# Kernel optimization log

Hardware: AMD Instinct MI355X
Metric: run time of the kernel (lower is better)

## Reference

```python
import jax, jax.numpy as jnp
import numpy as np

HIDDEN = 768
NUM_HEADS = 12
HEAD_DIM = HIDDEN // NUM_HEADS


def setup_inputs() -> dict:
    key = jax.random.key(0)
    ks = jax.random.split(key, 10)
    B, S = 4, 2048
    scale = 1.0 / np.sqrt(HIDDEN)
    inp = {
        "hidden_states": jax.random.normal(ks[0], (B, S, HIDDEN), dtype=jnp.float32),
        "attention_mask": jnp.ones((B, S), dtype=jnp.float32),
        "Wq": jax.random.normal(ks[1], (HIDDEN, HIDDEN), dtype=jnp.float32) * scale,
        "bq": jnp.zeros((HIDDEN,), dtype=jnp.float32),
        "Wk": jax.random.normal(ks[2], (HIDDEN, HIDDEN), dtype=jnp.float32) * scale,
        "bk": jnp.zeros((HIDDEN,), dtype=jnp.float32),
        "Wv": jax.random.normal(ks[3], (HIDDEN, HIDDEN), dtype=jnp.float32) * scale,
        "bv": jnp.zeros((HIDDEN,), dtype=jnp.float32),
        "Wo": jax.random.normal(ks[4], (HIDDEN, HIDDEN), dtype=jnp.float32) * scale,
        "bo": jnp.zeros((HIDDEN,), dtype=jnp.float32),
    }
    return inp


def _split_heads(x):
    # [B,S,H] -> [B,nh,S,dh]
    B, S, _ = x.shape
    return x.reshape(B, S, NUM_HEADS, HEAD_DIM).transpose(0, 2, 1, 3)


def reference(hidden_states, attention_mask, Wq, bq, Wk, bk, Wv, bv, Wo, bo):
    # Linear projections (torch nn.Linear: x @ W.T + b; here W stored as [in,out])
    q = _split_heads(hidden_states @ Wq + bq)
    k = _split_heads(hidden_states @ Wk + bk)
    v = _split_heads(hidden_states @ Wv + bv)

    # scores: [B,nh,S,S]
    scores = jnp.einsum("bhqd,bhkd->bhqk", q, k) / np.sqrt(HEAD_DIM).astype(np.float32)

    # outer-product mask: [B,1,S,S], broadcast over heads
    ext = (attention_mask[:, :, None] * attention_mask[:, None, :])[:, None, :, :]
    scores = ext * scores - (1.0 - ext) * 1e9

    probs = jax.nn.softmax(scores, axis=-1)
    ctx = jnp.einsum("bhqk,bhkd->bhqd", probs, v)  # [B,nh,S,dh]
    B, _, S, _ = ctx.shape
    ctx = ctx.transpose(0, 2, 1, 3).reshape(B, S, HIDDEN)
    out = ctx @ Wo + bo
    # torch F.gelu default: exact (erf-based)
    return jax.nn.gelu(out, approximate=False)
```

## Files before the change

kernel.cpp:

```cpp
#include <hip/hip_runtime.h>
#include <math.h>

#define HIDDEN 768
#define NH 12
#define DH 64
#define SEQ 2048
#define BATCH 4

typedef __bf16 bf16;
typedef bf16 bf16x4 __attribute__((ext_vector_type(4)));
typedef bf16 bf16x8 __attribute__((ext_vector_type(8)));
typedef float f32x4 __attribute__((ext_vector_type(4)));

__device__ __forceinline__ void load_lds16(const void* g, void* l) {
    __builtin_amdgcn_global_load_lds(
        (__attribute__((address_space(1))) void*)g,
        (__attribute__((address_space(3))) void*)l, 16, 0, 0);
}

__global__ __launch_bounds__(256) void prep_x(const float* __restrict__ X,
                                              bf16* __restrict__ Xb) {
    const size_t i = ((size_t)blockIdx.x * 256 + threadIdx.x) * 8;
    float4 a = *(const float4*)(X + i);
    float4 b = *(const float4*)(X + i + 4);
    bf16x8 o = {(bf16)a.x, (bf16)a.y, (bf16)a.z, (bf16)a.w,
                (bf16)b.x, (bf16)b.y, (bf16)b.z, (bf16)b.w};
    *(bf16x8*)(Xb + i) = o;
}

__global__ __launch_bounds__(256) void prep_w(const float* __restrict__ Wq,
                                              const float* __restrict__ Wk,
                                              const float* __restrict__ Wv,
                                              const float* __restrict__ Wo,
                                              bf16* __restrict__ Wt,
                                              bf16* __restrict__ Wot_hi,
                                              bf16* __restrict__ Wot_lo) {
    __shared__ float Ts[64][68];
    const int tid = threadIdx.x;
    const int n0 = blockIdx.x * 64, k0 = blockIdx.y * 64, z = blockIdx.z;
    const float* W = (z == 0) ? Wq : (z == 1) ? Wk : (z == 2) ? Wv : Wo;

    {
        const int r = tid >> 2, c = (tid & 3) << 4;
        const float* src = W + (size_t)(k0 + r) * HIDDEN + n0 + c;
#pragma unroll
        for (int j = 0; j < 4; ++j)
            *(float4*)&Ts[r][c + 4 * j] = *(const float4*)(src + 4 * j);
    }
    __syncthreads();

    const int nl = tid >> 2, kc = (tid & 3) << 4;
    float v[16];
#pragma unroll
    for (int j = 0; j < 16; ++j) v[j] = Ts[kc + j][nl];

    if (z < 3) {
        bf16 hi[16];
#pragma unroll
        for (int j = 0; j < 16; ++j) hi[j] = (bf16)v[j];
        const size_t off = (size_t)(z * HIDDEN + n0 + nl) * HIDDEN + k0 + kc;
        *(bf16x8*)(Wt + off) = *(bf16x8*)&hi[0];
        *(bf16x8*)(Wt + off + 8) = *(bf16x8*)&hi[8];
    } else {
        bf16 hi[16], lo[16];
#pragma unroll
        for (int j = 0; j < 16; ++j) {
            hi[j] = (bf16)v[j];
            lo[j] = (bf16)(v[j] - (float)hi[j]);
        }
        const size_t off = (size_t)(n0 + nl) * HIDDEN + k0 + kc;
        *(bf16x8*)(Wot_hi + off) = *(bf16x8*)&hi[0];
        *(bf16x8*)(Wot_hi + off + 8) = *(bf16x8*)&hi[8];
        *(bf16x8*)(Wot_lo + off) = *(bf16x8*)&lo[0];
        *(bf16x8*)(Wot_lo + off + 8) = *(bf16x8*)&lo[8];
    }
}

__global__ __launch_bounds__(256) void gemm_qkv(
    const bf16* __restrict__ Xb, const bf16* __restrict__ Wt,
    const float* __restrict__ bq, const float* __restrict__ bk,
    const float* __restrict__ bv, bf16* __restrict__ q_out,
    bf16* __restrict__ k_out, bf16* __restrict__ v_out) {
    __shared__ bf16 As[128 * 64];
    __shared__ bf16 Bs[128 * 64];

    const int tid = threadIdx.x;
    const int ln = tid & 63, wv = tid >> 6;
    const int quad = ln >> 4, l16 = ln & 15;
    const int wm = wv >> 1, wn = wv & 1;
    const int n0 = blockIdx.x * 128, m0 = blockIdx.y * 128;

    f32x4 acc[4][4];
#pragma unroll
    for (int i = 0; i < 4; ++i)
#pragma unroll
        for (int j = 0; j < 4; ++j) acc[i][j] = (f32x4){0.f, 0.f, 0.f, 0.f};

    const int r8 = ln >> 3;
    const int bcol_sw = ((ln & 7) << 4) ^ (r8 << 4);
    const char* gA =
        (const char*)Xb + ((size_t)(m0 + wv * 32 + r8) * HIDDEN) * 2 + bcol_sw;
    const char* gB =
        (const char*)Wt + ((size_t)(n0 + wv * 32 + r8) * HIDDEN) * 2 + bcol_sw;
    bf16* As_w = As + (wv * 32) * 64;
    bf16* Bs_w = Bs + (wv * 32) * 64;

    const int fsw = (l16 & 7) << 4;

    for (int k0 = 0; k0 < HIDDEN; k0 += 64) {
        __syncthreads();
#pragma unroll
        for (int j = 0; j < 4; ++j) {
            load_lds16(gA + (size_t)k0 * 2 + (size_t)j * (8 * HIDDEN * 2),
                       As_w + j * 8 * 64);
            load_lds16(gB + (size_t)k0 * 2 + (size_t)j * (8 * HIDDEN * 2),
                       Bs_w + j * 8 * 64);
        }
        __syncthreads();

        bf16x8 ah[4][2], bh[4][2];
#pragma unroll
        for (int i = 0; i < 4; ++i) {
            const char* ra = (const char*)As + (wm * 64 + i * 16 + l16) * 128;
            const char* rb = (const char*)Bs + (wn * 64 + i * 16 + l16) * 128;
            ah[i][0] = *(const bf16x8*)(ra + ((quad * 16) ^ fsw));
            ah[i][1] = *(const bf16x8*)(ra + ((64 + quad * 16) ^ fsw));
            bh[i][0] = *(const bf16x8*)(rb + ((quad * 16) ^ fsw));
            bh[i][1] = *(const bf16x8*)(rb + ((64 + quad * 16) ^ fsw));
        }
#pragma unroll
        for (int mi = 0; mi < 4; ++mi)
#pragma unroll
            for (int ni = 0; ni < 4; ++ni) {
                f32x4 c = acc[mi][ni];
                c = __builtin_amdgcn_mfma_f32_16x16x32_bf16(ah[mi][0], bh[ni][0],
                                                            c, 0, 0, 0);
                c = __builtin_amdgcn_mfma_f32_16x16x32_bf16(ah[mi][1], bh[ni][1],
                                                            c, 0, 0, 0);
                acc[mi][ni] = c;
            }
    }

    const int nb = n0 + wn * 64;
    const int which = nb / HIDDEN;
    const int nrel = nb - which * HIDDEN;
    const int h = nrel >> 6;

    if (which < 2) {
        const float scale = (which == 0) ? 0.18033688011112042f : 1.0f;
        const float* bias = (which == 0) ? bq : bk;
        bf16* dst = (which == 0) ? q_out : k_out;
#pragma unroll
        for (int ni = 0; ni < 4; ++ni) {
            const int dh = ni * 16 + l16;
            const float bb = bias[nrel + dh];
#pragma unroll
            for (int mi = 0; mi < 4; ++mi)
#pragma unroll
                for (int r = 0; r < 4; ++r) {
                    const int m = m0 + wm * 64 + mi * 16 + quad * 4 + r;
                    const int bi = m >> 11, s = m & (SEQ - 1);
                    dst[(((size_t)(bi * NH + h) * SEQ + s) << 6) + dh] =
                        (bf16)(scale * (acc[mi][ni][r] + bb));
                }
        }
    } else {
        const int bi = m0 >> 11;
        const int sbase = (m0 & (SEQ - 1)) + wm * 64;
#pragma unroll
        for (int ni = 0; ni < 4; ++ni) {
            const int dh = ni * 16 + l16;
            const float bb = bv[nrel + dh];
            bf16* vrow = v_out + ((size_t)(bi * NH + h) * DH + dh) * SEQ;
#pragma unroll
            for (int mi = 0; mi < 4; ++mi) {
                bf16x4 pk = {(bf16)(acc[mi][ni][0] + bb),
                             (bf16)(acc[mi][ni][1] + bb),
                             (bf16)(acc[mi][ni][2] + bb),
                             (bf16)(acc[mi][ni][3] + bb)};
                *(bf16x4*)(vrow + sbase + mi * 16 + quad * 4) = pk;
            }
        }
    }
}

__global__ __launch_bounds__(256) void attn_mfma(const bf16* __restrict__ Q,
                                                 const bf16* __restrict__ K,
                                                 const bf16* __restrict__ Vt,
                                                 const float* __restrict__ mask,
                                                 float* __restrict__ ctx) {
    __shared__ bf16 Ks[64 * 64];
    __shared__ bf16 Vts[64 * 64];
    __shared__ bf16 Ps[128 * 64];
    __shared__ float Ms[SEQ];
    __shared__ int allones_s;

    const int tid = threadIdx.x;
    const int ln = tid & 63, w = tid >> 6;
    const int quad = ln >> 4, l16 = ln & 15;

    const int wg = blockIdx.x;
    const int logical = (wg & 7) * 96 + (wg >> 3);
    const int qt = logical & 15;
    const int h = (logical >> 4) % NH;
    const int b = logical / (16 * NH);

    const size_t bh = (size_t)b * NH + h;
    const bf16* Qp = Q + ((bh * SEQ + (size_t)qt * 128) << 6);
    const bf16* Kp = K + (bh * SEQ << 6);
    const bf16* Vp = Vt + (bh * DH) * SEQ;

    if (tid == 0) allones_s = 1;
    {
        float4 m0 = *(const float4*)(mask + (size_t)b * SEQ + tid * 8);
        float4 m1 = *(const float4*)(mask + (size_t)b * SEQ + tid * 8 + 4);
        *(float4*)&Ms[tid * 8] = m0;
        *(float4*)&Ms[tid * 8 + 4] = m1;
        bool ok = (m0.x == 1.f) & (m0.y == 1.f) & (m0.z == 1.f) &
                  (m0.w == 1.f) & (m1.x == 1.f) & (m1.y == 1.f) &
                  (m1.z == 1.f) & (m1.w == 1.f);
        __syncthreads();
        if (!ok) allones_s = 0;
    }
    __syncthreads();
    const bool fastmask = (allones_s != 0);

    bf16x8 qb[2][2];
#pragma unroll
    for (int qg = 0; qg < 2; ++qg)
#pragma unroll
        for (int hf = 0; hf < 2; ++hf)
            qb[qg][hf] = *(const bf16x8*)(Qp + ((w * 32 + qg * 16 + l16) << 6) +
                                          hf * 32 + quad * 8);
    float mq[2];
#pragma unroll
    for (int qg = 0; qg < 2; ++qg)
        mq[qg] = Ms[qt * 128 + w * 32 + qg * 16 + l16];

    float l_i[2] = {0.f, 0.f};
    f32x4 acc[4][2];
#pragma unroll
    for (int fd = 0; fd < 4; ++fd)
#pragma unroll
        for (int qg = 0; qg < 2; ++qg) acc[fd][qg] = (f32x4){0.f, 0.f, 0.f, 0.f};

    const int sr = tid >> 2, sc = (tid & 3) << 4;
    const int ssw = (sr & 7) << 3;
    const int d0 = sc ^ ssw, d1 = (sc + 8) ^ ssw;
    const bf16* kbase = Kp + ((size_t)sr << 6) + sc;
    const bf16* vbase = Vp + (size_t)sr * SEQ + sc;

    bf16x8 kr0, kr1, vr0, vr1;
    kr0 = *(const bf16x8*)kbase;
    kr1 = *(const bf16x8*)(kbase + 8);
    vr0 = *(const bf16x8*)vbase;
    vr1 = *(const bf16x8*)(vbase + 8);

    for (int kt = 0; kt < SEQ / 64; ++kt) {
        __syncthreads();
        *(bf16x8*)&Ks[sr * 64 + d0] = kr0;
        *(bf16x8*)&Ks[sr * 64 + d1] = kr1;
        *(bf16x8*)&Vts[sr * 64 + d0] = vr0;
        *(bf16x8*)&Vts[sr * 64 + d1] = vr1;
        __syncthreads();
        if (kt + 1 < SEQ / 64) {
            kr0 = *(const bf16x8*)(kbase + ((size_t)(kt + 1) << 12));
            kr1 = *(const bf16x8*)(kbase + ((size_t)(kt + 1) << 12) + 8);
            vr0 = *(const bf16x8*)(vbase + (kt + 1) * 64);
            vr1 = *(const bf16x8*)(vbase + (kt + 1) * 64 + 8);
        }

        const int fsw = (l16 & 7) << 3;
        f32x4 st[4][2];
#pragma unroll
        for (int f = 0; f < 4; ++f) {
            const int krow = (f * 16 + l16) * 64;
            bf16x8 ka0 = *(bf16x8*)&Ks[krow + ((quad * 8) ^ fsw)];
            bf16x8 ka1 = *(bf16x8*)&Ks[krow + ((32 + quad * 8) ^ fsw)];
#pragma unroll
            for (int qg = 0; qg < 2; ++qg) {
                f32x4 c = {0.f, 0.f, 0.f, 0.f};
                c = __builtin_amdgcn_mfma_f32_16x16x32_bf16(ka0, qb[qg][0], c, 0, 0, 0);
                c = __builtin_amdgcn_mfma_f32_16x16x32_bf16(ka1, qb[qg][1], c, 0, 0, 0);
                st[f][qg] = c;
            }
        }

        if (!fastmask) {
#pragma unroll
            for (int f = 0; f < 4; ++f) {
                const float4 mk4 = *(const float4*)&Ms[kt * 64 + f * 16 + quad * 4];
                const float mkk[4] = {mk4.x, mk4.y, mk4.z, mk4.w};
#pragma unroll
                for (int qg = 0; qg < 2; ++qg)
#pragma unroll
                    for (int r = 0; r < 4; ++r) {
                        const float ext = mq[qg] * mkk[r];
                        st[f][qg][r] =
                            ext * st[f][qg][r] - (1.0f - ext) * 1.4426950e9f;
                    }
            }
        }

#pragma unroll
        for (int qg = 0; qg < 2; ++qg) {
            const int row = w * 32 + qg * 16 + l16;
            const int sw = (row & 7) << 3;
            bf16* prow = &Ps[row * 64];
#pragma unroll
            for (int f = 0; f < 4; ++f) {
                float p0 = __builtin_amdgcn_exp2f(st[f][qg][0]);
                float p1 = __builtin_amdgcn_exp2f(st[f][qg][1]);
                float p2 = __builtin_amdgcn_exp2f(st[f][qg][2]);
                float p3 = __builtin_amdgcn_exp2f(st[f][qg][3]);
                l_i[qg] += (p0 + p1) + (p2 + p3);
                bf16x4 pk = {(bf16)p0, (bf16)p1, (bf16)p2, (bf16)p3};
                *(bf16x4*)&prow[(f * 16 + quad * 4) ^ sw] = pk;
            }
        }

        bf16x8 pb[2][2];
#pragma unroll
        for (int qg = 0; qg < 2; ++qg) {
            const int row = w * 32 + qg * 16 + l16;
            const int sw = (row & 7) << 3;
#pragma unroll
            for (int hf = 0; hf < 2; ++hf)
                pb[qg][hf] =
                    *(bf16x8*)&Ps[row * 64 + ((hf * 32 + quad * 8) ^ sw)];
        }
#pragma unroll
        for (int fd = 0; fd < 4; ++fd) {
            const int vrow = (fd * 16 + l16) * 64;
            bf16x8 va0 = *(bf16x8*)&Vts[vrow + ((quad * 8) ^ fsw)];
            bf16x8 va1 = *(bf16x8*)&Vts[vrow + ((32 + quad * 8) ^ fsw)];
#pragma unroll
            for (int qg = 0; qg < 2; ++qg) {
                f32x4 c = acc[fd][qg];
                c = __builtin_amdgcn_mfma_f32_16x16x32_bf16(va0, pb[qg][0], c, 0, 0, 0);
                c = __builtin_amdgcn_mfma_f32_16x16x32_bf16(va1, pb[qg][1], c, 0, 0, 0);
                acc[fd][qg] = c;
            }
        }
    }

#pragma unroll
    for (int qg = 0; qg < 2; ++qg) {
        l_i[qg] += __shfl_xor(l_i[qg], 16);
        l_i[qg] += __shfl_xor(l_i[qg], 32);
    }

#pragma unroll
    for (int qg = 0; qg < 2; ++qg) {
        const float inv = 1.0f / l_i[qg];
        const size_t row = (size_t)b * SEQ + qt * 128 + w * 32 + qg * 16 + l16;
#pragma unroll
        for (int fd = 0; fd < 4; ++fd) {
            float4 o = {acc[fd][qg][0] * inv, acc[fd][qg][1] * inv,
                        acc[fd][qg][2] * inv, acc[fd][qg][3] * inv};
            *(float4*)(ctx + row * HIDDEN + h * 64 + fd * 16 + quad * 4) = o;
        }
    }
}

__global__ __launch_bounds__(256) void gemm_out(const float* __restrict__ ctx,
                                                const bf16* __restrict__ Bhi,
                                                const bf16* __restrict__ Blo,
                                                const float* __restrict__ bo,
                                                float* __restrict__ fout) {
    __shared__ bf16 As_hi[128][40];
    __shared__ bf16 As_lo[128][40];
    __shared__ bf16 Bs_hi[64][40];
    __shared__ bf16 Bs_lo[64][40];

    const int tid = threadIdx.x;
    const int ln = tid & 63, wv = tid >> 6;
    const int quad = ln >> 4, l16 = ln & 15;
    const int wm = wv >> 1, wn = wv & 1;
    const int n0 = blockIdx.x * 64, m0 = blockIdx.y * 128;

    f32x4 acc[4][2];
#pragma unroll
    for (int i = 0; i < 4; ++i)
#pragma unroll
        for (int j = 0; j < 2; ++j) acc[i][j] = (f32x4){0.f, 0.f, 0.f, 0.f};

    const int sra = tid >> 1, sca = (tid & 1) << 4;
    const int srb = tid >> 2, scb = (tid & 3) << 3;
    const float* gA = ctx + (size_t)(m0 + sra) * HIDDEN + sca;
    const bf16* gBh = Bhi + (size_t)(n0 + srb) * HIDDEN + scb;
    const bf16* gBl = Blo + (size_t)(n0 + srb) * HIDDEN + scb;

    float fa[16];
    bf16x8 brh, brl;
#pragma unroll
    for (int j = 0; j < 4; ++j) *(float4*)&fa[4 * j] = *(const float4*)(gA + 4 * j);
    brh = *(const bf16x8*)gBh;
    brl = *(const bf16x8*)gBl;

    for (int k0 = 0; k0 < HIDDEN; k0 += 32) {
        bf16 hi[16], lo[16];
#pragma unroll
        for (int j = 0; j < 16; ++j) {
            hi[j] = (bf16)fa[j];
            lo[j] = (bf16)(fa[j] - (float)hi[j]);
        }
        __syncthreads();
        *(bf16x8*)&As_hi[sra][sca] = *(bf16x8*)&hi[0];
        *(bf16x8*)&As_hi[sra][sca + 8] = *(bf16x8*)&hi[8];
        *(bf16x8*)&As_lo[sra][sca] = *(bf16x8*)&lo[0];
        *(bf16x8*)&As_lo[sra][sca + 8] = *(bf16x8*)&lo[8];
        *(bf16x8*)&Bs_hi[srb][scb] = brh;
        *(bf16x8*)&Bs_lo[srb][scb] = brl;
        __syncthreads();
        if (k0 + 32 < HIDDEN) {
#pragma unroll
            for (int j = 0; j < 4; ++j)
                *(float4*)&fa[4 * j] = *(const float4*)(gA + k0 + 32 + 4 * j);
            brh = *(const bf16x8*)(gBh + k0 + 32);
            brl = *(const bf16x8*)(gBl + k0 + 32);
        }

        bf16x8 ah[4], al[4], bh[2], bl[2];
#pragma unroll
        for (int i = 0; i < 4; ++i) {
            ah[i] = *(bf16x8*)&As_hi[wm * 64 + i * 16 + l16][quad * 8];
            al[i] = *(bf16x8*)&As_lo[wm * 64 + i * 16 + l16][quad * 8];
        }
#pragma unroll
        for (int i = 0; i < 2; ++i) {
            bh[i] = *(bf16x8*)&Bs_hi[wn * 32 + i * 16 + l16][quad * 8];
            bl[i] = *(bf16x8*)&Bs_lo[wn * 32 + i * 16 + l16][quad * 8];
        }
#pragma unroll
        for (int mi = 0; mi < 4; ++mi)
#pragma unroll
            for (int ni = 0; ni < 2; ++ni) {
                f32x4 c = acc[mi][ni];
                c = __builtin_amdgcn_mfma_f32_16x16x32_bf16(ah[mi], bh[ni], c, 0, 0, 0);
                c = __builtin_amdgcn_mfma_f32_16x16x32_bf16(ah[mi], bl[ni], c, 0, 0, 0);
                c = __builtin_amdgcn_mfma_f32_16x16x32_bf16(al[mi], bh[ni], c, 0, 0, 0);
                acc[mi][ni] = c;
            }
    }

#pragma unroll
    for (int ni = 0; ni < 2; ++ni) {
        const int n = n0 + wn * 32 + ni * 16 + l16;
        const float bb = bo[n];
#pragma unroll
        for (int mi = 0; mi < 4; ++mi)
#pragma unroll
            for (int r = 0; r < 4; ++r) {
                const int m = m0 + wm * 64 + mi * 16 + quad * 4 + r;
                float x = acc[mi][ni][r] + bb;
                x = 0.5f * x * (1.0f + erff(x * 0.70710678118654752440f));
                fout[(size_t)m * HIDDEN + n] = x;
            }
    }
}

extern "C" void kernel_launch(void* const* d_in, const int* in_sizes, int n_in,
                              void* d_out, int out_size, void* d_ws, size_t ws_size,
                              hipStream_t stream) {
    const float* X    = (const float*)d_in[0];
    const float* mask = (const float*)d_in[1];
    const float* Wq   = (const float*)d_in[2];
    const float* bq   = (const float*)d_in[3];
    const float* Wk   = (const float*)d_in[4];
    const float* bk   = (const float*)d_in[5];
    const float* Wv   = (const float*)d_in[6];
    const float* bv   = (const float*)d_in[7];
    const float* Wo   = (const float*)d_in[8];
    const float* bo   = (const float*)d_in[9];
    float* out = (float*)d_out;

    char* w = (char*)d_ws;
    const size_t NE = (size_t)BATCH * SEQ * HIDDEN;
    bf16* q_ws   = (bf16*)w;  w += NE * 2;
    bf16* k_ws   = (bf16*)w;  w += NE * 2;
    bf16* vt_ws  = (bf16*)w;  w += NE * 2;
    float* ctx   = (float*)w; w += NE * 4;
    bf16* Xb     = (bf16*)w;  w += NE * 2;
    bf16* Wt     = (bf16*)w;  w += (size_t)3 * HIDDEN * HIDDEN * 2;
    bf16* Wot_hi = (bf16*)w;  w += (size_t)HIDDEN * HIDDEN * 2;
    bf16* Wot_lo = (bf16*)w;  w += (size_t)HIDDEN * HIDDEN * 2;

    prep_x<<<(int)(NE / 2048), 256, 0, stream>>>(X, Xb);
    prep_w<<<dim3(12, 12, 4), 256, 0, stream>>>(Wq, Wk, Wv, Wo, Wt, Wot_hi,
                                                Wot_lo);
    gemm_qkv<<<dim3(18, 64), 256, 0, stream>>>(Xb, Wt, bq, bk, bv, q_ws, k_ws,
                                               vt_ws);
    attn_mfma<<<dim3(16 * NH * BATCH), 256, 0, stream>>>(q_ws, k_ws, vt_ws,
                                                         mask, ctx);
    gemm_out<<<dim3(12, 64), 256, 0, stream>>>(ctx, Wot_hi, Wot_lo, bo, out);
}
```

Measured before the change: 263.1 us.

## Emit bf16 hi/lo context from attention and stream gemm_out via direct LDS loads

The attention kernel now splits its fp32 context output into bf16 hi and lo halves in its epilogue, so the output GEMM no longer converts fp32 on every K step. gemm_out is restructured to use global_load_lds into XOR-swizzled 64-wide K tiles, halving the number of K iterations and barriers and removing register staging. The workspace footprint is unchanged (two bf16 arrays replace one fp32 array). The trade-off is the loss of the register prefetch overlap, since loads are issued and then waited on inside each iteration with no double buffering.

```diff
diff --git a/kernel.cpp b/kernel.cpp
--- a/kernel.cpp
+++ b/kernel.cpp
@@ -188,7 +188,8 @@
                                                  const bf16* __restrict__ K,
                                                  const bf16* __restrict__ Vt,
                                                  const float* __restrict__ mask,
-                                                 float* __restrict__ ctx) {
+                                                 bf16* __restrict__ ctx_hi,
+                                                 bf16* __restrict__ ctx_lo) {
     __shared__ bf16 Ks[64 * 64];
     __shared__ bf16 Vts[64 * 64];
     __shared__ bf16 Ps[128 * 64];
@@ -356,22 +357,30 @@
         const size_t row = (size_t)b * SEQ + qt * 128 + w * 32 + qg * 16 + l16;
 #pragma unroll
         for (int fd = 0; fd < 4; ++fd) {
-            float4 o = {acc[fd][qg][0] * inv, acc[fd][qg][1] * inv,
-                        acc[fd][qg][2] * inv, acc[fd][qg][3] * inv};
-            *(float4*)(ctx + row * HIDDEN + h * 64 + fd * 16 + quad * 4) = o;
-        }
-    }
-}
-
-__global__ __launch_bounds__(256) void gemm_out(const float* __restrict__ ctx,
+            bf16 hi[4], lo[4];
+#pragma unroll
+            for (int r = 0; r < 4; ++r) {
+                const float o = acc[fd][qg][r] * inv;
+                hi[r] = (bf16)o;
+                lo[r] = (bf16)(o - (float)hi[r]);
+            }
+            const size_t off = row * HIDDEN + h * 64 + fd * 16 + quad * 4;
+            *(bf16x4*)(ctx_hi + off) = *(bf16x4*)&hi[0];
+            *(bf16x4*)(ctx_lo + off) = *(bf16x4*)&lo[0];
+        }
+    }
+}
+
+__global__ __launch_bounds__(256) void gemm_out(const bf16* __restrict__ Ah,
+                                                const bf16* __restrict__ Al,
                                                 const bf16* __restrict__ Bhi,
                                                 const bf16* __restrict__ Blo,
                                                 const float* __restrict__ bo,
                                                 float* __restrict__ fout) {
-    __shared__ bf16 As_hi[128][40];
-    __shared__ bf16 As_lo[128][40];
-    __shared__ bf16 Bs_hi[64][40];
-    __shared__ bf16 Bs_lo[64][40];
+    __shared__ bf16 As_hi[128 * 64];
+    __shared__ bf16 As_lo[128 * 64];
+    __shared__ bf16 Bs_hi[64 * 64];
+    __shared__ bf16 Bs_lo[64 * 64];
 
     const int tid = threadIdx.x;
     const int ln = tid & 63, wv = tid >> 6;
@@ -385,63 +394,75 @@
 #pragma unroll
         for (int j = 0; j < 2; ++j) acc[i][j] = (f32x4){0.f, 0.f, 0.f, 0.f};
 
-    const int sra = tid >> 1, sca = (tid & 1) << 4;
-    const int srb = tid >> 2, scb = (tid & 3) << 3;
-    const float* gA = ctx + (size_t)(m0 + sra) * HIDDEN + sca;
-    const bf16* gBh = Bhi + (size_t)(n0 + srb) * HIDDEN + scb;
-    const bf16* gBl = Blo + (size_t)(n0 + srb) * HIDDEN + scb;
-
-    float fa[16];
-    bf16x8 brh, brl;
-#pragma unroll
-    for (int j = 0; j < 4; ++j) *(float4*)&fa[4 * j] = *(const float4*)(gA + 4 * j);
-    brh = *(const bf16x8*)gBh;
-    brl = *(const bf16x8*)gBl;
-
-    for (int k0 = 0; k0 < HIDDEN; k0 += 32) {
-        bf16 hi[16], lo[16];
-#pragma unroll
-        for (int j = 0; j < 16; ++j) {
-            hi[j] = (bf16)fa[j];
-            lo[j] = (bf16)(fa[j] - (float)hi[j]);
-        }
-        __syncthreads();
-        *(bf16x8*)&As_hi[sra][sca] = *(bf16x8*)&hi[0];
-        *(bf16x8*)&As_hi[sra][sca + 8] = *(bf16x8*)&hi[8];
-        *(bf16x8*)&As_lo[sra][sca] = *(bf16x8*)&lo[0];
-        *(bf16x8*)&As_lo[sra][sca + 8] = *(bf16x8*)&lo[8];
-        *(bf16x8*)&Bs_hi[srb][scb] = brh;
-        *(bf16x8*)&Bs_lo[srb][scb] = brl;
-        __syncthreads();
-        if (k0 + 32 < HIDDEN) {
-#pragma unroll
-            for (int j = 0; j < 4; ++j)
-                *(float4*)&fa[4 * j] = *(const float4*)(gA + k0 + 32 + 4 * j);
-            brh = *(const bf16x8*)(gBh + k0 + 32);
-            brl = *(const bf16x8*)(gBl + k0 + 32);
-        }
-
-        bf16x8 ah[4], al[4], bh[2], bl[2];
-#pragma unroll
-        for (int i = 0; i < 4; ++i) {
-            ah[i] = *(bf16x8*)&As_hi[wm * 64 + i * 16 + l16][quad * 8];
-            al[i] = *(bf16x8*)&As_lo[wm * 64 + i * 16 + l16][quad * 8];
-        }
-#pragma unroll
-        for (int i = 0; i < 2; ++i) {
-            bh[i] = *(bf16x8*)&Bs_hi[wn * 32 + i * 16 + l16][quad * 8];
-            bl[i] = *(bf16x8*)&Bs_lo[wn * 32 + i * 16 + l16][quad * 8];
-        }
-#pragma unroll
-        for (int mi = 0; mi < 4; ++mi)
-#pragma unroll
-            for (int ni = 0; ni < 2; ++ni) {
-                f32x4 c = acc[mi][ni];
-                c = __builtin_amdgcn_mfma_f32_16x16x32_bf16(ah[mi], bh[ni], c, 0, 0, 0);
-                c = __builtin_amdgcn_mfma_f32_16x16x32_bf16(ah[mi], bl[ni], c, 0, 0, 0);
-                c = __builtin_amdgcn_mfma_f32_16x16x32_bf16(al[mi], bh[ni], c, 0, 0, 0);
-                acc[mi][ni] = c;
-            }
+    const int r8 = ln >> 3;
+    const int bcol_sw = ((ln & 7) << 4) ^ (r8 << 4);
+    const char* gAh =
+        (const char*)Ah + ((size_t)(m0 + wv * 32 + r8) * HIDDEN) * 2 + bcol_sw;
+    const char* gAl =
+        (const char*)Al + ((size_t)(m0 + wv * 32 + r8) * HIDDEN) * 2 + bcol_sw;
+    const char* gBh =
+        (const char*)Bhi + ((size_t)(n0 + wv * 16 + r8) * HIDDEN) * 2 + bcol_sw;
+    const char* gBl =
+        (const char*)Blo + ((size_t)(n0 + wv * 16 + r8) * HIDDEN) * 2 + bcol_sw;
+    bf16* Ash_w = As_hi + (wv * 32) * 64;
+    bf16* Asl_w = As_lo + (wv * 32) * 64;
+    bf16* Bsh_w = Bs_hi + (wv * 16) * 64;
+    bf16* Bsl_w = Bs_lo + (wv * 16) * 64;
+
+    const int fsw = (l16 & 7) << 4;
+
+    for (int k0 = 0; k0 < HIDDEN; k0 += 64) {
+        __syncthreads();
+#pragma unroll
+        for (int j = 0; j < 4; ++j) {
+            load_lds16(gAh + (size_t)k0 * 2 + (size_t)j * (8 * HIDDEN * 2),
+                       Ash_w + j * 8 * 64);
+            load_lds16(gAl + (size_t)k0 * 2 + (size_t)j * (8 * HIDDEN * 2),
+                       Asl_w + j * 8 * 64);
+        }
+#pragma unroll
+        for (int j = 0; j < 2; ++j) {
+            load_lds16(gBh + (size_t)k0 * 2 + (size_t)j * (8 * HIDDEN * 2),
+                       Bsh_w + j * 8 * 64);
+            load_lds16(gBl + (size_t)k0 * 2 + (size_t)j * (8 * HIDDEN * 2),
+                       Bsl_w + j * 8 * 64);
+        }
+        __syncthreads();
+
+#pragma unroll
+        for (int kk = 0; kk < 2; ++kk) {
+            const int kb = kk * 64;
+            bf16x8 ah[4], al[4], bh[2], bl[2];
+#pragma unroll
+            for (int i = 0; i < 4; ++i) {
+                const int row = (wm * 64 + i * 16 + l16) * 128;
+                ah[i] = *(const bf16x8*)((const char*)As_hi + row +
+                                         ((kb + quad * 16) ^ fsw));
+                al[i] = *(const bf16x8*)((const char*)As_lo + row +
+                                         ((kb + quad * 16) ^ fsw));
+            }
+#pragma unroll
+            for (int i = 0; i < 2; ++i) {
+                const int row = (wn * 32 + i * 16 + l16) * 128;
+                bh[i] = *(const bf16x8*)((const char*)Bs_hi + row +
+                                         ((kb + quad * 16) ^ fsw));
+                bl[i] = *(const bf16x8*)((const char*)Bs_lo + row +
+                                         ((kb + quad * 16) ^ fsw));
+            }
+#pragma unroll
+            for (int mi = 0; mi < 4; ++mi)
+#pragma unroll
+                for (int ni = 0; ni < 2; ++ni) {
+                    f32x4 c = acc[mi][ni];
+                    c = __builtin_amdgcn_mfma_f32_16x16x32_bf16(ah[mi], bh[ni],
+                                                                c, 0, 0, 0);
+                    c = __builtin_amdgcn_mfma_f32_16x16x32_bf16(ah[mi], bl[ni],
+                                                                c, 0, 0, 0);
+                    c = __builtin_amdgcn_mfma_f32_16x16x32_bf16(al[mi], bh[ni],
+                                                                c, 0, 0, 0);
+                    acc[mi][ni] = c;
+                }
+        }
     }
 
 #pragma unroll
@@ -480,7 +501,8 @@
     bf16* q_ws   = (bf16*)w;  w += NE * 2;
     bf16* k_ws   = (bf16*)w;  w += NE * 2;
     bf16* vt_ws  = (bf16*)w;  w += NE * 2;
-    float* ctx   = (float*)w; w += NE * 4;
+    bf16* ctx_hi = (bf16*)w;  w += NE * 2;
+    bf16* ctx_lo = (bf16*)w;  w += NE * 2;
     bf16* Xb     = (bf16*)w;  w += NE * 2;
     bf16* Wt     = (bf16*)w;  w += (size_t)3 * HIDDEN * HIDDEN * 2;
     bf16* Wot_hi = (bf16*)w;  w += (size_t)HIDDEN * HIDDEN * 2;
@@ -491,7 +513,8 @@
                                                 Wot_lo);
     gemm_qkv<<<dim3(18, 64), 256, 0, stream>>>(Xb, Wt, bq, bk, bv, q_ws, k_ws,
                                                vt_ws);
-    attn_mfma<<<dim3(16 * NH * BATCH), 256, 0, stream>>>(q_ws, k_ws, vt_ws,
-                                                         mask, ctx);
-    gemm_out<<<dim3(12, 64), 256, 0, stream>>>(ctx, Wot_hi, Wot_lo, bo, out);
-}
+    attn_mfma<<<dim3(16 * NH * BATCH), 256, 0, stream>>>(
+        q_ws, k_ws, vt_ws, mask, ctx_hi, ctx_lo);
+    gemm_out<<<dim3(12, 64), 256, 0, stream>>>(ctx_hi, ctx_lo, Wot_hi, Wot_lo,
+                                               bo, out);
+}
```

After: 264.2 us. Within noise of the previous version (+0.4%).
